# Performance work log

Hardware: AMD Instinct MI355X
Metric: run time of the kernel (lower is better)

The kernel has to match this reference:

```python
import jax, jax.numpy as jnp
import numpy as np

ALPHA = 1.0

def setup_inputs() -> dict:
    key = jax.random.key(0)
    kx, kc = jax.random.split(key)
    x = jax.random.normal(kx, (2048, 128, 32), dtype=jnp.float32)      # (N, T, F)
    clusters = jax.random.normal(kc, (32, 128, 32), dtype=jnp.float32)  # (K, T, F)
    return {"x": x, "clusters": clusters}

def reference(x, clusters):
    # Euclidean-over-time distance per feature:
    #   ed[n,k,f] = sqrt(sum_t (x[n,t,f] - c[k,t,f])^2)
    # computed via the expanded quadratic form to avoid the (N,K,T,F) broadcast.
    x2 = jnp.sum(x * x, axis=1)               # (N, F)
    c2 = jnp.sum(clusters * clusters, axis=1)  # (K, F)
    xc = jnp.einsum('ntf,ktf->nkf', x, clusters)  # (N, K, F)
    sq = x2[:, None, :] + c2[None, :, :] - 2.0 * xc
    ed = jnp.sqrt(jnp.maximum(sq, 0.0))        # (N, K, F)
    distance = jnp.sum(ed, axis=-1)            # (N, K)
    # Student's t soft assignment
    q = 1.0 / (1.0 + (distance * distance) / ALPHA)
    q = q ** ((ALPHA + 1.0) / 2.0)
    q = q / jnp.sum(q, axis=1, keepdims=True)
    return q
```

## Files before the change

kernel.cpp:

```cpp
#include <hip/hip_runtime.h>


#define T_DIM 128
#define F_DIM 32
#define K_DIM 32
#define TF (T_DIM * F_DIM)

__global__ __launch_bounds__(256, 1) void tscluster_kernel(
    const float* __restrict__ x,
    const float* __restrict__ c,
    float* __restrict__ out)
{
    const int tid   = threadIdx.x;
    const int f_grp = tid & 7;
    const int k_grp = (tid >> 3) & 7;
    const int n_grp = tid >> 6;
    const int f0 = f_grp << 2;
    const int k0 = k_grp << 2;
    const int n0 = (blockIdx.x << 3) + (n_grp << 1);

    const float* xp0 = x + (size_t)n0 * TF + f0;
    const float* xp1 = xp0 + TF;
    const float* cp0 = c + (size_t)k0 * TF + f0;
    const float* cp1 = cp0 + TF;
    const float* cp2 = cp1 + TF;
    const float* cp3 = cp2 + TF;

    float acc[2][4][4];
    #pragma unroll
    for (int a = 0; a < 2; ++a)
        #pragma unroll
        for (int b = 0; b < 4; ++b)
            #pragma unroll
            for (int j = 0; j < 4; ++j)
                acc[a][b][j] = 0.0f;

    #pragma unroll 2
    for (int t = 0; t < T_DIM; ++t) {
        const int off = t * F_DIM;
        const float4 xv0 = *reinterpret_cast<const float4*>(xp0 + off);
        const float4 xv1 = *reinterpret_cast<const float4*>(xp1 + off);
        const float4 cv0 = *reinterpret_cast<const float4*>(cp0 + off);
        const float4 cv1 = *reinterpret_cast<const float4*>(cp1 + off);
        const float4 cv2 = *reinterpret_cast<const float4*>(cp2 + off);
        const float4 cv3 = *reinterpret_cast<const float4*>(cp3 + off);

        const float xs0[4] = {xv0.x, xv0.y, xv0.z, xv0.w};
        const float xs1[4] = {xv1.x, xv1.y, xv1.z, xv1.w};
        const float cs[4][4] = {
            {cv0.x, cv0.y, cv0.z, cv0.w},
            {cv1.x, cv1.y, cv1.z, cv1.w},
            {cv2.x, cv2.y, cv2.z, cv2.w},
            {cv3.x, cv3.y, cv3.z, cv3.w},
        };

        #pragma unroll
        for (int kk = 0; kk < 4; ++kk) {
            #pragma unroll
            for (int j = 0; j < 4; ++j) {
                const float d0 = xs0[j] - cs[kk][j];
                acc[0][kk][j] += d0 * d0;
                const float d1 = xs1[j] - cs[kk][j];
                acc[1][kk][j] += d1 * d1;
            }
        }
    }

    float dist[2][4];
    #pragma unroll
    for (int a = 0; a < 2; ++a)
        #pragma unroll
        for (int b = 0; b < 4; ++b)
            dist[a][b] = sqrtf(acc[a][b][0]) + sqrtf(acc[a][b][1]) +
                         sqrtf(acc[a][b][2]) + sqrtf(acc[a][b][3]);

    #pragma unroll
    for (int off = 1; off < 8; off <<= 1) {
        #pragma unroll
        for (int a = 0; a < 2; ++a)
            #pragma unroll
            for (int b = 0; b < 4; ++b)
                dist[a][b] += __shfl_xor(dist[a][b], off, 64);
    }

    float qun[2][4];
    float qs[2];
    #pragma unroll
    for (int a = 0; a < 2; ++a) {
        qs[a] = 0.0f;
        #pragma unroll
        for (int b = 0; b < 4; ++b) {
            qun[a][b] = 1.0f / (1.0f + dist[a][b] * dist[a][b]);
            qs[a] += qun[a][b];
        }
    }

    #pragma unroll
    for (int off = 8; off < 64; off <<= 1) {
        #pragma unroll
        for (int a = 0; a < 2; ++a)
            qs[a] += __shfl_xor(qs[a], off, 64);
    }

    if (f_grp == 0) {
        #pragma unroll
        for (int a = 0; a < 2; ++a) {
            float4 qv;
            qv.x = qun[a][0] / qs[a];
            qv.y = qun[a][1] / qs[a];
            qv.z = qun[a][2] / qs[a];
            qv.w = qun[a][3] / qs[a];
            *reinterpret_cast<float4*>(out + (size_t)(n0 + a) * K_DIM + k0) = qv;
        }
    }
}

extern "C" void kernel_launch(void* const* d_in, const int* in_sizes, int n_in,
                              void* d_out, int out_size, void* d_ws, size_t ws_size,
                              hipStream_t stream) {
    const float* x = (const float*)d_in[0];
    const float* c = (const float*)d_in[1];
    float* out = (float*)d_out;
    tscluster_kernel<<<dim3(256), dim3(256), 0, stream>>>(x, c, out);
}
```

Baseline: 100.0 us.

## Replace direct distance loop with bf16 MFMA quadratic-form pipeline

```diff
diff --git a/kernel.cpp b/kernel.cpp
--- a/kernel.cpp
+++ b/kernel.cpp
@@ -1,118 +1,136 @@
 #include <hip/hip_runtime.h>
+#include <hip/hip_bf16.h>
 
 
-#define T_DIM 128
-#define F_DIM 32
-#define K_DIM 32
-#define TF (T_DIM * F_DIM)
+typedef __attribute__((ext_vector_type(8)))  short  short8;
+typedef __attribute__((ext_vector_type(16))) float  float16;
 
-__global__ __launch_bounds__(256, 1) void tscluster_kernel(
-    const float* __restrict__ x,
-    const float* __restrict__ c,
-    float* __restrict__ out)
+#define NTOT 2048
+#define TDIM 128
+#define FDIM 32
+#define KDIM 32
+
+#define OFF_XT   0
+#define OFF_CT   16777216
+#define OFF_X2   17039360
+#define OFF_C2   17301504
+#define OFF_PART 17305600
+
+__global__ __launch_bounds__(256) void transpose_pack_kernel(
+    const float* __restrict__ src,
+    unsigned short* __restrict__ dstT,
+    float* __restrict__ dst2,
+    int Rtot)
 {
-    const int tid   = threadIdx.x;
-    const int f_grp = tid & 7;
-    const int k_grp = (tid >> 3) & 7;
-    const int n_grp = tid >> 6;
-    const int f0 = f_grp << 2;
-    const int k0 = k_grp << 2;
-    const int n0 = (blockIdx.x << 3) + (n_grp << 1);
+    __shared__ unsigned short lds[8 * 128 * 32];
+    const int tid = threadIdx.x;
+    const int r0 = blockIdx.x * 8;
 
-    const float* xp0 = x + (size_t)n0 * TF + f0;
-    const float* xp1 = xp0 + TF;
-    const float* cp0 = c + (size_t)k0 * TF + f0;
-    const float* cp1 = cp0 + TF;
-    const float* cp2 = cp1 + TF;
-    const float* cp3 = cp2 + TF;
+    const float* sp = src + (size_t)r0 * (TDIM * FDIM);
+    #pragma unroll
+    for (int i = 0; i < 32; ++i) {
+        const float4 v = *reinterpret_cast<const float4*>(sp + ((size_t)i * 256 + tid) * 4);
+        union { __hip_bfloat16 h; unsigned short u; } c0, c1, c2, c3;
+        c0.h = __float2bfloat16(v.x); c1.h = __float2bfloat16(v.y);
+        c2.h = __float2bfloat16(v.z); c3.h = __float2bfloat16(v.w);
+        uint2 pk;
+        pk.x = (unsigned)c0.u | ((unsigned)c1.u << 16);
+        pk.y = (unsigned)c2.u | ((unsigned)c3.u << 16);
+        *reinterpret_cast<uint2*>(&lds[((size_t)i * 256 + tid) * 4]) = pk;
+    }
+    __syncthreads();
 
-    float acc[2][4][4];
+    const int f = tid & 31, nl = tid >> 5;
+    const int rg = r0 + nl;
+    float x2 = 0.f;
+    unsigned short* op = dstT + ((size_t)f * Rtot + rg) * TDIM;
+    #pragma unroll 4
+    for (int t8 = 0; t8 < 16; ++t8) {
+        uint4 ow;
+        unsigned* owp = reinterpret_cast<unsigned*>(&ow);
+        #pragma unroll
+        for (int p = 0; p < 4; ++p) {
+            const unsigned short ua = lds[(nl * 128 + t8 * 8 + p * 2    ) * 32 + f];
+            const unsigned short ub = lds[(nl * 128 + t8 * 8 + p * 2 + 1) * 32 + f];
+            const float fa = __uint_as_float((unsigned)ua << 16);
+            const float fb = __uint_as_float((unsigned)ub << 16);
+            x2 = fmaf(fa, fa, x2);
+            x2 = fmaf(fb, fb, x2);
+            owp[p] = (unsigned)ua | ((unsigned)ub << 16);
+        }
+        *reinterpret_cast<uint4*>(op + t8 * 8) = ow;
+    }
+    dst2[(size_t)f * Rtot + rg] = x2;
+}
+
+__global__ __launch_bounds__(512, 2) void xc_mfma_kernel(
+    const unsigned short* __restrict__ xT,
+    const unsigned short* __restrict__ cT,
+    const float* __restrict__ x2T,
+    const float* __restrict__ c2T,
+    float* __restrict__ part)
+{
+    __shared__ float dist[1024];
+    const int tid = threadIdx.x;
+    const int l = tid & 63, w = tid >> 6;
+    const int nt = blockIdx.x & 63, fg = blockIdx.x >> 6;
+    const int n0 = nt * 32;
+    const int f  = fg * 8 + w;
+
+    if (tid < 256) reinterpret_cast<float4*>(dist)[tid] = make_float4(0.f, 0.f, 0.f, 0.f);
+    __syncthreads();
+
+    const int m = l & 31, g = l >> 5;
+    const unsigned short* ap = xT + ((size_t)f * NTOT + (n0 + m)) * TDIM + g * 8;
+    const unsigned short* bp = cT + ((size_t)f * KDIM + m) * TDIM + g * 8;
+
+    short8 av[8], bv[8];
     #pragma unroll
-    for (int a = 0; a < 2; ++a)
-        #pragma unroll
-        for (int b = 0; b < 4; ++b)
-            #pragma unroll
-            for (int j = 0; j < 4; ++j)
-                acc[a][b][j] = 0.0f;
-
-    #pragma unroll 2
-    for (int t = 0; t < T_DIM; ++t) {
-        const int off = t * F_DIM;
-        const float4 xv0 = *reinterpret_cast<const float4*>(xp0 + off);
-        const float4 xv1 = *reinterpret_cast<const float4*>(xp1 + off);
-        const float4 cv0 = *reinterpret_cast<const float4*>(cp0 + off);
-        const float4 cv1 = *reinterpret_cast<const float4*>(cp1 + off);
-        const float4 cv2 = *reinterpret_cast<const float4*>(cp2 + off);
-        const float4 cv3 = *reinterpret_cast<const float4*>(cp3 + off);
-
-        const float xs0[4] = {xv0.x, xv0.y, xv0.z, xv0.w};
-        const float xs1[4] = {xv1.x, xv1.y, xv1.z, xv1.w};
-        const float cs[4][4] = {
-            {cv0.x, cv0.y, cv0.z, cv0.w},
-            {cv1.x, cv1.y, cv1.z, cv1.w},
-            {cv2.x, cv2.y, cv2.z, cv2.w},
-            {cv3.x, cv3.y, cv3.z, cv3.w},
-        };
-
-        #pragma unroll
-        for (int kk = 0; kk < 4; ++kk) {
-            #pragma unroll
-            for (int j = 0; j < 4; ++j) {
-                const float d0 = xs0[j] - cs[kk][j];
-                acc[0][kk][j] += d0 * d0;
-                const float d1 = xs1[j] - cs[kk][j];
-                acc[1][kk][j] += d1 * d1;
-            }
-        }
+    for (int c = 0; c < 8; ++c) {
+        av[c] = *reinterpret_cast<const short8*>(ap + c * 16);
+        bv[c] = *reinterpret_cast<const short8*>(bp + c * 16);
     }
 
-    float dist[2][4];
+    float16 acc;
     #pragma unroll
-    for (int a = 0; a < 2; ++a)
-        #pragma unroll
-        for (int b = 0; b < 4; ++b)
-            dist[a][b] = sqrtf(acc[a][b][0]) + sqrtf(acc[a][b][1]) +
-                         sqrtf(acc[a][b][2]) + sqrtf(acc[a][b][3]);
+    for (int r = 0; r < 16; ++r) acc[r] = 0.f;
+    #pragma unroll
+    for (int c = 0; c < 8; ++c)
+        acc = __builtin_amdgcn_mfma_f32_32x32x16_bf16(av[c], bv[c], acc, 0, 0, 0);
 
+    const float c2v = c2T[f * KDIM + m];
     #pragma unroll
-    for (int off = 1; off < 8; off <<= 1) {
-        #pragma unroll
-        for (int a = 0; a < 2; ++a)
-            #pragma unroll
-            for (int b = 0; b < 4; ++b)
-                dist[a][b] += __shfl_xor(dist[a][b], off, 64);
+    for (int r = 0; r < 16; ++r) {
+        const int rm = (r & 3) + 8 * (r >> 2) + 4 * g;
+        const float x2v = x2T[(size_t)f * NTOT + n0 + rm];
+        const float sq = x2v + c2v - 2.0f * acc[r];
+        const float ed = sqrtf(fmaxf(sq, 0.0f));
+        atomicAdd(&dist[rm * 32 + m], ed);
     }
+    __syncthreads();
 
-    float qun[2][4];
-    float qs[2];
+    float* pb = part + (size_t)fg * (NTOT * KDIM) + (size_t)n0 * KDIM;
+    pb[tid]       = dist[tid];
+    pb[tid + 512] = dist[tid + 512];
+}
+
+__global__ __launch_bounds__(256) void qnorm_kernel(
+    const float* __restrict__ part, float* __restrict__ out)
+{
+    const int tid = threadIdx.x;
+    const int l = tid & 63, wv = tid >> 6;
+    const int n = blockIdx.x * 8 + wv * 2 + (l >> 5);
+    const int k = l & 31;
+    const size_t idx = (size_t)n * KDIM + k;
+    const float d = part[idx]
+                  + part[idx + 1 * NTOT * KDIM]
+                  + part[idx + 2 * NTOT * KDIM]
+                  + part[idx + 3 * NTOT * KDIM];
+    const float qun = 1.0f / (1.0f + d * d);
+    float s = qun;
     #pragma unroll
-    for (int a = 0; a < 2; ++a) {
-        qs[a] = 0.0f;
-        #pragma unroll
-        for (int b = 0; b < 4; ++b) {
-            qun[a][b] = 1.0f / (1.0f + dist[a][b] * dist[a][b]);
-            qs[a] += qun[a][b];
-        }
-    }
-
-    #pragma unroll
-    for (int off = 8; off < 64; off <<= 1) {
-        #pragma unroll
-        for (int a = 0; a < 2; ++a)
-            qs[a] += __shfl_xor(qs[a], off, 64);
-    }
-
-    if (f_grp == 0) {
-        #pragma unroll
-        for (int a = 0; a < 2; ++a) {
-            float4 qv;
-            qv.x = qun[a][0] / qs[a];
-            qv.y = qun[a][1] / qs[a];
-            qv.z = qun[a][2] / qs[a];
-            qv.w = qun[a][3] / qs[a];
-            *reinterpret_cast<float4*>(out + (size_t)(n0 + a) * K_DIM + k0) = qv;
-        }
-    }
+    for (int off = 1; off < 32; off <<= 1) s += __shfl_xor(s, off, 64);
+    out[idx] = qun / s;
 }
 
 extern "C" void kernel_launch(void* const* d_in, const int* in_sizes, int n_in,
@@ -121,5 +139,16 @@
     const float* x = (const float*)d_in[0];
     const float* c = (const float*)d_in[1];
     float* out = (float*)d_out;
-    tscluster_kernel<<<dim3(256), dim3(256), 0, stream>>>(x, c, out);
+    char* ws = (char*)d_ws;
+
+    unsigned short* xT  = (unsigned short*)(ws + OFF_XT);
+    unsigned short* cT  = (unsigned short*)(ws + OFF_CT);
+    float*          x2T = (float*)(ws + OFF_X2);
+    float*          c2T = (float*)(ws + OFF_C2);
+    float*          prt = (float*)(ws + OFF_PART);
+
+    transpose_pack_kernel<<<dim3(NTOT / 8), dim3(256), 0, stream>>>(x, xT, x2T, NTOT);
+    transpose_pack_kernel<<<dim3(KDIM / 8), dim3(256), 0, stream>>>(c, cT, c2T, KDIM);
+    xc_mfma_kernel<<<dim3(256), dim3(512), 0, stream>>>(xT, cT, x2T, c2T, prt);
+    qnorm_kernel<<<dim3(NTOT / 8), dim3(256), 0, stream>>>(prt, out);
 }
```

Result: slower. 104.0 us (+4.0%).
